# Kernel optimization log

Hardware: AMD Instinct MI355X
Metric: run time of the kernel (lower is better)

The kernel has to match this reference:

```python
import jax, jax.numpy as jnp
import numpy as np

N = 50000        # nodes
E = 800000       # edges (avg degree 16)
F_IN = 256       # cfg.dataset.features
H = 256          # cfg.model.hidden_size


def setup_inputs() -> dict:
    key = jax.random.key(0)
    ks = jax.random.split(key, 8)
    x = jax.random.normal(ks[0], (N, F_IN), dtype=jnp.float32)
    edge_index = jax.random.randint(ks[1], (2, E), 0, N, dtype=jnp.int32)
    # GCNConv weights: layer0 in->hidden, layer1 hidden->hidden, layer2 hidden->1
    W0 = jax.random.normal(ks[2], (F_IN, H), jnp.float32) / np.sqrt(F_IN)
    b0 = jnp.zeros((H,), jnp.float32)
    W1 = jax.random.normal(ks[3], (H, H), jnp.float32) / np.sqrt(H)
    b1 = jnp.zeros((H,), jnp.float32)
    W2 = jax.random.normal(ks[4], (H, 1), jnp.float32) / np.sqrt(H)
    b2 = jnp.zeros((1,), jnp.float32)
    return {"x": x, "edge_index": edge_index, "W0": W0, "b0": b0,
            "W1": W1, "b1": b1, "W2": W2, "b2": b2}


def reference(x, edge_index, W0, b0, W1, b1, W2, b2):
    n = x.shape[0]
    loop = jnp.arange(n, dtype=edge_index.dtype)
    # gcn_norm with self-loops: Ahat = D^{-1/2} (A + I) D^{-1/2}
    src = jnp.concatenate([edge_index[0], loop])  # [E+N]
    dst = jnp.concatenate([edge_index[1], loop])  # [E+N]
    deg = jax.ops.segment_sum(jnp.ones_like(src, dtype=x.dtype), dst, num_segments=n)
    dinv = jnp.where(deg > 0, jax.lax.rsqrt(deg), 0.0)
    norm = dinv[src] * dinv[dst]                  # [E+N]

    def gcn_layer(h, W, b):
        h = h @ W                                              # [N, out]
        agg = jax.ops.segment_sum(norm[:, None] * h[src], dst, num_segments=n)
        return agg + b

    h = jax.nn.relu(gcn_layer(x, W0, b0))
    h = jax.nn.relu(gcn_layer(h, W1, b1))
    return gcn_layer(h, W2, b2)                                # [N, 1]
```

## Files before the change

### kernel.cpp

```cpp
#include <hip/hip_runtime.h>


static inline size_t alignup(size_t x, size_t a) { return (x + a - 1) & ~(a - 1); }

typedef __attribute__((ext_vector_type(8))) short short8;
typedef __attribute__((ext_vector_type(4))) float f32x4;

__device__ inline unsigned short f2bf(float f) {
    union { float f; unsigned int u; } v; v.f = f;
    unsigned int r = v.u + 0x7FFFu + ((v.u >> 16) & 1u);
    return (unsigned short)(r >> 16);
}
__device__ inline float bf2f(unsigned short u) {
    union { unsigned int u; float f; } v; v.u = ((unsigned int)u) << 16;
    return v.f;
}

__global__ __launch_bounds__(256) void k_fill_i32(int* __restrict__ p, int v, int n) {
    int i = blockIdx.x * 256 + threadIdx.x;
    if (i < n) p[i] = v;
}

__global__ __launch_bounds__(256) void k_count_deg(const int* __restrict__ dst, int* __restrict__ deg, int E) {
    int e = blockIdx.x * 256 + threadIdx.x;
    if (e < E) atomicAdd(&deg[dst[e]], 1);
}

__global__ __launch_bounds__(256) void k_scan1(const int* __restrict__ deg, int* __restrict__ rs,
                                               int* __restrict__ bsum, float* __restrict__ dinv, int n) {
    __shared__ int sd[256];
    int b = blockIdx.x, tid = threadIdx.x;
    int base = b * 1024 + tid * 4;
    int v[4];
#pragma unroll
    for (int j = 0; j < 4; ++j) v[j] = (base + j < n) ? deg[base + j] : 0;
    int tot = v[0] + v[1] + v[2] + v[3];
    sd[tid] = tot;
    for (int off = 1; off < 256; off <<= 1) {
        __syncthreads();
        int t = (tid >= off) ? sd[tid - off] : 0;
        __syncthreads();
        sd[tid] += t;
    }
    __syncthreads();
    int run = tid ? sd[tid - 1] : 0;
#pragma unroll
    for (int j = 0; j < 4; ++j) {
        if (base + j < n) {
            rs[base + j] = run;
            dinv[base + j] = rsqrtf((float)v[j] + 1.0f);
        }
        run += v[j];
    }
    if (tid == 255) bsum[b] = sd[255];
}

__global__ __launch_bounds__(256) void k_scan2(int* __restrict__ bsum, int nb) {
    __shared__ int sd[256];
    int tid = threadIdx.x;
    sd[tid] = (tid < nb) ? bsum[tid] : 0;
    for (int off = 1; off < 256; off <<= 1) {
        __syncthreads();
        int t = (tid >= off) ? sd[tid - off] : 0;
        __syncthreads();
        sd[tid] += t;
    }
    __syncthreads();
    if (tid < nb) bsum[tid] = tid ? sd[tid - 1] : 0;
}

__global__ __launch_bounds__(256) void k_scan3(int* __restrict__ rs, int* __restrict__ cursor,
                                               const int* __restrict__ bsum, int n, int E) {
    int b = blockIdx.x, tid = threadIdx.x;
    int off = bsum[b];
    int base = b * 1024 + tid * 4;
#pragma unroll
    for (int j = 0; j < 4; ++j) {
        int idx = base + j;
        if (idx < n) {
            int v = rs[idx] + off;
            rs[idx] = v;
            cursor[idx] = v;
        }
    }
    if (b == 0 && tid == 0) rs[n] = E;
}

__global__ __launch_bounds__(256) void k_fill_csr(const int* __restrict__ src, const int* __restrict__ dst,
                                                  int* __restrict__ cursor, int* __restrict__ col, int E) {
    int e = blockIdx.x * 256 + threadIdx.x;
    if (e < E) {
        int d = dst[e];
        int pos = atomicAdd(&cursor[d], 1);
        col[pos] = src[e];
    }
}

__global__ __launch_bounds__(256) void k_wt2(const float* __restrict__ W0, const float* __restrict__ W1,
                                             unsigned short* __restrict__ Wt0, unsigned short* __restrict__ Wt1) {
    int idx = blockIdx.x * 256 + threadIdx.x;
    const float* W = (idx < 65536) ? W0 : W1;
    unsigned short* Wt = (idx < 65536) ? Wt0 : Wt1;
    int id = idx & 65535;
    int k = id >> 8, n = id & 255;
    Wt[(size_t)n * 256 + k] = f2bf(W[(size_t)k * 256 + n]);
}

__global__ __launch_bounds__(256) void k_xb(const float* __restrict__ x, unsigned short* __restrict__ xb,
                                            int total8) {
    int i = blockIdx.x * 256 + threadIdx.x;
    if (i >= total8) return;
    float4 f0 = *(const float4*)(x + (size_t)i * 8);
    float4 f1 = *(const float4*)(x + (size_t)i * 8 + 4);
    short8 u;
    u[0] = (short)f2bf(f0.x); u[1] = (short)f2bf(f0.y);
    u[2] = (short)f2bf(f0.z); u[3] = (short)f2bf(f0.w);
    u[4] = (short)f2bf(f1.x); u[5] = (short)f2bf(f1.y);
    u[6] = (short)f2bf(f1.z); u[7] = (short)f2bf(f1.w);
    *(short8*)(xb + (size_t)i * 8) = u;
}

__global__ __launch_bounds__(256) void k_gemm_mfma(const unsigned short* __restrict__ A,
                                                   const unsigned short* __restrict__ Wt,
                                                   unsigned short* __restrict__ C,
                                                   const float* __restrict__ dinv, int N) {
    __shared__ __align__(16) unsigned short As2[128 * 32];
    __shared__ __align__(16) unsigned short Bs2[128 * 32];
    __shared__ __align__(16) unsigned short Cs[4 * 64 * 64];

    int tid = threadIdx.x;
    int lane = tid & 63, w = tid >> 6;
    int wr = w >> 1, wc = w & 1;
    int row0 = blockIdx.y * 128, col0 = blockIdx.x * 128;

    f32x4 acc[4][4];
#pragma unroll
    for (int m = 0; m < 4; ++m)
#pragma unroll
        for (int n = 0; n < 4; ++n) acc[m][n] = (f32x4)0.f;

    for (int k0 = 0; k0 < 256; k0 += 32) {
#pragma unroll
        for (int it = 0; it < 2; ++it) {
            int c = tid + it * 256;
            int r = c >> 2, kg = c & 3;
            int grow = row0 + r;
            short8 u = {0, 0, 0, 0, 0, 0, 0, 0};
            if (grow < N) u = *(const short8*)(A + (size_t)grow * 256 + k0 + kg * 8);
            *(short8*)&As2[(r >> 4) * 512 + kg * 128 + (r & 15) * 8] = u;
        }
#pragma unroll
        for (int it = 0; it < 2; ++it) {
            int c = tid + it * 256;
            int n = c >> 2, kg = c & 3;
            short8 u = *(const short8*)(Wt + (size_t)(col0 + n) * 256 + k0 + kg * 8);
            *(short8*)&Bs2[(n >> 4) * 512 + kg * 128 + (n & 15) * 8] = u;
        }
        __syncthreads();
        short8 af[4], bfr[4];
#pragma unroll
        for (int m = 0; m < 4; ++m)
            af[m] = *(const short8*)&As2[(wr * 4 + m) * 512 + (lane >> 4) * 128 + (lane & 15) * 8];
#pragma unroll
        for (int n = 0; n < 4; ++n)
            bfr[n] = *(const short8*)&Bs2[(wc * 4 + n) * 512 + (lane >> 4) * 128 + (lane & 15) * 8];
#pragma unroll
        for (int m = 0; m < 4; ++m)
#pragma unroll
            for (int n = 0; n < 4; ++n)
                acc[m][n] = __builtin_amdgcn_mfma_f32_16x16x32_bf16(af[m], bfr[n], acc[m][n], 0, 0, 0);
        __syncthreads();
    }

    unsigned short* myCs = &Cs[w * 4096];
#pragma unroll
    for (int m = 0; m < 4; ++m) {
#pragma unroll
        for (int j = 0; j < 4; ++j) {
            int r = m * 16 + (lane >> 4) * 4 + j;
            int grow = row0 + wr * 64 + r;
            float d = (grow < N) ? dinv[grow] : 0.f;
#pragma unroll
            for (int n = 0; n < 4; ++n)
                myCs[r * 64 + n * 16 + (lane & 15)] = f2bf(acc[m][n][j] * d);
        }
    }
    __syncthreads();
#pragma unroll
    for (int i = 0; i < 8; ++i) {
        int r = i * 8 + (lane >> 3);
        int grow = row0 + wr * 64 + r;
        if (grow < N) {
            short8 v = *(const short8*)&myCs[r * 64 + (lane & 7) * 8];
            *(short8*)(C + (size_t)grow * 256 + col0 + wc * 64 + (lane & 7) * 8) = v;
        }
    }
}

__global__ __launch_bounds__(256) void k_agg(const unsigned short* __restrict__ t,
                                             unsigned short* __restrict__ h,
                                             const int* __restrict__ rs, const int* __restrict__ col,
                                             const float* __restrict__ dinv, const float* __restrict__ bias,
                                             int N, int do_relu) {
    int wid = (blockIdx.x * 256 + threadIdx.x) >> 6;
    int lane = threadIdx.x & 63;
    if (wid >= N) return;
    int half = lane >> 5, sub = lane & 31;
    const short8* tp = (const short8*)t;

    short8 sv = tp[(size_t)wid * 32 + sub];
    float hsel = (half == 0) ? 1.f : 0.f;
    float a[8];
#pragma unroll
    for (int i = 0; i < 8; ++i) a[i] = hsel * bf2f((unsigned short)sv[i]);

    int e0 = rs[wid], e1 = rs[wid + 1];
    for (int base = e0; base < e1; base += 64) {
        int m = e1 - base; if (m > 64) m = 64;
        int c = (base + lane < e1) ? col[base + lane] : 0;
        int npairs = (m + 1) >> 1;
        int j = 0;
        for (; j + 4 <= npairs; j += 4) {
            int i0 = 2 * j + half, i1 = i0 + 2, i2 = i0 + 4, i3 = i0 + 6;
            int s0 = __shfl(c, i0), s1 = __shfl(c, i1), s2 = __shfl(c, i2), s3 = __shfl(c, i3);
            float f0 = (i0 < m) ? 1.f : 0.f, f1 = (i1 < m) ? 1.f : 0.f;
            float f2 = (i2 < m) ? 1.f : 0.f, f3 = (i3 < m) ? 1.f : 0.f;
            short8 w0 = tp[(size_t)s0 * 32 + sub];
            short8 w1 = tp[(size_t)s1 * 32 + sub];
            short8 w2 = tp[(size_t)s2 * 32 + sub];
            short8 w3 = tp[(size_t)s3 * 32 + sub];
#pragma unroll
            for (int i = 0; i < 8; ++i) {
                a[i] = fmaf(f0, bf2f((unsigned short)w0[i]), a[i]);
                a[i] = fmaf(f1, bf2f((unsigned short)w1[i]), a[i]);
                a[i] = fmaf(f2, bf2f((unsigned short)w2[i]), a[i]);
                a[i] = fmaf(f3, bf2f((unsigned short)w3[i]), a[i]);
            }
        }
        for (; j < npairs; ++j) {
            int i0 = 2 * j + half;
            int s0 = __shfl(c, i0);
            float f0 = (i0 < m) ? 1.f : 0.f;
            short8 w0 = tp[(size_t)s0 * 32 + sub];
#pragma unroll
            for (int i = 0; i < 8; ++i) a[i] = fmaf(f0, bf2f((unsigned short)w0[i]), a[i]);
        }
    }
#pragma unroll
    for (int i = 0; i < 8; ++i) a[i] += __shfl_xor(a[i], 32, 64);

    if (half == 0) {
        float d = dinv[wid];
        float4 b0 = ((const float4*)bias)[sub * 2];
        float4 b1 = ((const float4*)bias)[sub * 2 + 1];
        float o[8];
        o[0] = fmaf(d, a[0], b0.x); o[1] = fmaf(d, a[1], b0.y);
        o[2] = fmaf(d, a[2], b0.z); o[3] = fmaf(d, a[3], b0.w);
        o[4] = fmaf(d, a[4], b1.x); o[5] = fmaf(d, a[5], b1.y);
        o[6] = fmaf(d, a[6], b1.z); o[7] = fmaf(d, a[7], b1.w);
        short8 u;
#pragma unroll
        for (int i = 0; i < 8; ++i) {
            float v = do_relu ? fmaxf(o[i], 0.f) : o[i];
            u[i] = (short)f2bf(v);
        }
        *(short8*)(h + (size_t)wid * 256 + sub * 8) = u;
    }
}

__global__ __launch_bounds__(256) void k_gemv(const unsigned short* __restrict__ h, const float* __restrict__ w,
                                              const float* __restrict__ dinv, float* __restrict__ z, int N) {
    int wid = (blockIdx.x * 256 + threadIdx.x) >> 6;
    int lane = threadIdx.x & 63;
    if (wid >= N) return;
    ushort4 hv = ((const ushort4*)(h + (size_t)wid * 256))[lane];
    float4 wv = ((const float4*)w)[lane];
    float s = bf2f(hv.x) * wv.x + bf2f(hv.y) * wv.y + bf2f(hv.z) * wv.z + bf2f(hv.w) * wv.w;
#pragma unroll
    for (int off = 32; off > 0; off >>= 1) s += __shfl_down(s, off, 64);
    if (lane == 0) z[wid] = dinv[wid] * s;
}

__global__ __launch_bounds__(256) void k_agg_out(const float* __restrict__ z, float* __restrict__ out,
                                                 const int* __restrict__ rs, const int* __restrict__ col,
                                                 const float* __restrict__ dinv, const float* __restrict__ b2,
                                                 int N) {
    int wid = (blockIdx.x * 256 + threadIdx.x) >> 6;
    int lane = threadIdx.x & 63;
    if (wid >= N) return;
    int e0 = rs[wid], e1 = rs[wid + 1];
    float v = 0.f;
    for (int base = e0; base < e1; base += 64) {
        int e = base + lane;
        if (e < e1) v += z[col[e]];
    }
#pragma unroll
    for (int off = 32; off > 0; off >>= 1) v += __shfl_down(v, off, 64);
    if (lane == 0) out[wid] = fmaf(dinv[wid], v + z[wid], b2[0]);
}

extern "C" void kernel_launch(void* const* d_in, const int* in_sizes, int n_in,
                              void* d_out, int out_size, void* d_ws, size_t ws_size,
                              hipStream_t stream) {
    const float* x  = (const float*)d_in[0];
    const int*   ei = (const int*)d_in[1];
    const float* W0 = (const float*)d_in[2];
    const float* b0 = (const float*)d_in[3];
    const float* W1 = (const float*)d_in[4];
    const float* b1 = (const float*)d_in[5];
    const float* W2 = (const float*)d_in[6];
    const float* b2 = (const float*)d_in[7];
    float* out = (float*)d_out;

    int N = in_sizes[0] / 256;
    int E = in_sizes[1] / 2;
    const int* esrc = ei;
    const int* edst = ei + E;

    char* p = (char*)d_ws;
    unsigned short* tb = (unsigned short*)p; p += alignup((size_t)N * 256 * 2, 16);
    unsigned short* hb = (unsigned short*)p; p += alignup((size_t)N * 256 * 2, 16);
    unsigned short* xb = (unsigned short*)p; p += alignup((size_t)N * 256 * 2, 16);
    unsigned short* Wt0 = (unsigned short*)p; p += 256 * 256 * 2;
    unsigned short* Wt1 = (unsigned short*)p; p += 256 * 256 * 2;
    float* z = (float*)p;      p += alignup((size_t)N * 4, 16);
    float* dinv = (float*)p;   p += alignup((size_t)N * 4, 16);
    int* deg = (int*)p;        p += alignup((size_t)N * 4, 16);
    int* cursor = (int*)p;     p += alignup((size_t)N * 4, 16);
    int* rs = (int*)p;         p += alignup((size_t)(N + 1) * 4, 16);
    int* col = (int*)p;        p += alignup((size_t)E * 4, 16);
    int* bsum = (int*)p;       p += 256 * 4;

    int nb = (N + 1023) / 1024;
    dim3 blk(256);

    k_fill_i32<<<(N + 255) / 256, blk, 0, stream>>>(deg, 0, N);
    k_count_deg<<<(E + 255) / 256, blk, 0, stream>>>(edst, deg, E);
    k_scan1<<<nb, blk, 0, stream>>>(deg, rs, bsum, dinv, N);
    k_scan2<<<1, blk, 0, stream>>>(bsum, nb);
    k_scan3<<<nb, blk, 0, stream>>>(rs, cursor, bsum, N, E);
    k_fill_csr<<<(E + 255) / 256, blk, 0, stream>>>(esrc, edst, cursor, col, E);
    k_wt2<<<512, blk, 0, stream>>>(W0, W1, Wt0, Wt1);
    int total8 = N * 32;
    k_xb<<<(total8 + 255) / 256, blk, 0, stream>>>(x, xb, total8);

    dim3 gg(2, (N + 127) / 128);
    k_gemm_mfma<<<gg, blk, 0, stream>>>(xb, Wt0, tb, dinv, N);
    k_agg<<<(N + 3) / 4, blk, 0, stream>>>(tb, hb, rs, col, dinv, b0, N, 1);
    k_gemm_mfma<<<gg, blk, 0, stream>>>(hb, Wt1, tb, dinv, N);
    k_agg<<<(N + 3) / 4, blk, 0, stream>>>(tb, hb, rs, col, dinv, b1, N, 1);
    k_gemv<<<(N + 3) / 4, blk, 0, stream>>>(hb, W2, dinv, z, N);
    k_agg_out<<<(N + 3) / 4, blk, 0, stream>>>(z, out, rs, col, dinv, b2, N);
}
```

Before: 384.8 us.

## Fuse x bf16 conversion into GEMM, prefetch K tiles, fuse GEMV into aggregation

The separate fp32-to-bf16 conversion kernel is removed; the first GEMM now reads fp32 x and converts it while loading. The GEMM loop prefetches the next K tile into registers during the MFMA work and reuses one shared buffer for staging and output. The second aggregation computes the final 256->1 projection in place, so the second hidden activation is never written and the separate GEMV kernel goes away. This removes a full N×256 bf16 write and read pair plus two launches, at the cost of more registers and an extra barrier per K step.

```diff
diff --git a/kernel.cpp b/kernel.cpp
--- a/kernel.cpp
+++ b/kernel.cpp
@@ -106,27 +106,15 @@
     Wt[(size_t)n * 256 + k] = f2bf(W[(size_t)k * 256 + n]);
 }
 
-__global__ __launch_bounds__(256) void k_xb(const float* __restrict__ x, unsigned short* __restrict__ xb,
-                                            int total8) {
-    int i = blockIdx.x * 256 + threadIdx.x;
-    if (i >= total8) return;
-    float4 f0 = *(const float4*)(x + (size_t)i * 8);
-    float4 f1 = *(const float4*)(x + (size_t)i * 8 + 4);
-    short8 u;
-    u[0] = (short)f2bf(f0.x); u[1] = (short)f2bf(f0.y);
-    u[2] = (short)f2bf(f0.z); u[3] = (short)f2bf(f0.w);
-    u[4] = (short)f2bf(f1.x); u[5] = (short)f2bf(f1.y);
-    u[6] = (short)f2bf(f1.z); u[7] = (short)f2bf(f1.w);
-    *(short8*)(xb + (size_t)i * 8) = u;
-}
-
-__global__ __launch_bounds__(256) void k_gemm_mfma(const unsigned short* __restrict__ A,
+template <bool AF32>
+__global__ __launch_bounds__(256) void k_gemm_mfma(const void* __restrict__ Ap,
                                                    const unsigned short* __restrict__ Wt,
                                                    unsigned short* __restrict__ C,
                                                    const float* __restrict__ dinv, int N) {
-    __shared__ __align__(16) unsigned short As2[128 * 32];
-    __shared__ __align__(16) unsigned short Bs2[128 * 32];
-    __shared__ __align__(16) unsigned short Cs[4 * 64 * 64];
+    __shared__ __align__(16) unsigned short smem[16384];
+    unsigned short* As2 = smem;
+    unsigned short* Bs2 = smem + 4096;
+    unsigned short* Cs = smem;
 
     int tid = threadIdx.x;
     int lane = tid & 63, w = tid >> 6;
@@ -139,24 +127,52 @@
 #pragma unroll
         for (int n = 0; n < 4; ++n) acc[m][n] = (f32x4)0.f;
 
-    for (int k0 = 0; k0 < 256; k0 += 32) {
-#pragma unroll
-        for (int it = 0; it < 2; ++it) {
-            int c = tid + it * 256;
-            int r = c >> 2, kg = c & 3;
-            int grow = row0 + r;
-            short8 u = {0, 0, 0, 0, 0, 0, 0, 0};
-            if (grow < N) u = *(const short8*)(A + (size_t)grow * 256 + k0 + kg * 8);
-            *(short8*)&As2[(r >> 4) * 512 + kg * 128 + (r & 15) * 8] = u;
-        }
-#pragma unroll
-        for (int it = 0; it < 2; ++it) {
-            int c = tid + it * 256;
-            int n = c >> 2, kg = c & 3;
-            short8 u = *(const short8*)(Wt + (size_t)(col0 + n) * 256 + k0 + kg * 8);
-            *(short8*)&Bs2[(n >> 4) * 512 + kg * 128 + (n & 15) * 8] = u;
-        }
-        __syncthreads();
+    const int c0 = tid, c1 = tid + 256;
+    const int ar0 = c0 >> 2, akg0 = c0 & 3, ar1 = c1 >> 2, akg1 = c1 & 3;
+
+    auto loadA = [&](int r, int kg, int k0) -> short8 {
+        short8 u = {0, 0, 0, 0, 0, 0, 0, 0};
+        int grow = row0 + r;
+        if (grow < N) {
+            if constexpr (AF32) {
+                const float* g = (const float*)Ap + (size_t)grow * 256 + k0 + kg * 8;
+                float4 f0 = *(const float4*)g;
+                float4 f1 = *(const float4*)(g + 4);
+                u[0] = (short)f2bf(f0.x); u[1] = (short)f2bf(f0.y);
+                u[2] = (short)f2bf(f0.z); u[3] = (short)f2bf(f0.w);
+                u[4] = (short)f2bf(f1.x); u[5] = (short)f2bf(f1.y);
+                u[6] = (short)f2bf(f1.z); u[7] = (short)f2bf(f1.w);
+            } else {
+                u = *(const short8*)((const unsigned short*)Ap + (size_t)grow * 256 + k0 + kg * 8);
+            }
+        }
+        return u;
+    };
+    auto loadB = [&](int n, int kg, int k0) -> short8 {
+        return *(const short8*)(Wt + (size_t)(col0 + n) * 256 + k0 + kg * 8);
+    };
+    auto stash = [&](short8 a0, short8 a1, short8 b0, short8 b1) {
+        *(short8*)&As2[(ar0 >> 4) * 512 + akg0 * 128 + (ar0 & 15) * 8] = a0;
+        *(short8*)&As2[(ar1 >> 4) * 512 + akg1 * 128 + (ar1 & 15) * 8] = a1;
+        *(short8*)&Bs2[(ar0 >> 4) * 512 + akg0 * 128 + (ar0 & 15) * 8] = b0;
+        *(short8*)&Bs2[(ar1 >> 4) * 512 + akg1 * 128 + (ar1 & 15) * 8] = b1;
+    };
+
+    {
+        short8 a0 = loadA(ar0, akg0, 0), a1 = loadA(ar1, akg1, 0);
+        short8 b0 = loadB(ar0, akg0, 0), b1 = loadB(ar1, akg1, 0);
+        stash(a0, a1, b0, b1);
+    }
+    __syncthreads();
+
+#pragma unroll
+    for (int i = 0; i < 8; ++i) {
+        short8 na0, na1, nb0, nb1;
+        if (i < 7) {
+            int k0 = i * 32 + 32;
+            na0 = loadA(ar0, akg0, k0); na1 = loadA(ar1, akg1, k0);
+            nb0 = loadB(ar0, akg0, k0); nb1 = loadB(ar1, akg1, k0);
+        }
         short8 af[4], bfr[4];
 #pragma unroll
         for (int m = 0; m < 4; ++m)
@@ -169,8 +185,13 @@
 #pragma unroll
             for (int n = 0; n < 4; ++n)
                 acc[m][n] = __builtin_amdgcn_mfma_f32_16x16x32_bf16(af[m], bfr[n], acc[m][n], 0, 0, 0);
-        __syncthreads();
-    }
+        if (i < 7) {
+            __syncthreads();
+            stash(na0, na1, nb0, nb1);
+            __syncthreads();
+        }
+    }
+    __syncthreads();
 
     unsigned short* myCs = &Cs[w * 4096];
 #pragma unroll
@@ -197,11 +218,13 @@
     }
 }
 
+template <bool FUSE_GEMV>
 __global__ __launch_bounds__(256) void k_agg(const unsigned short* __restrict__ t,
                                              unsigned short* __restrict__ h,
                                              const int* __restrict__ rs, const int* __restrict__ col,
                                              const float* __restrict__ dinv, const float* __restrict__ bias,
-                                             int N, int do_relu) {
+                                             const float* __restrict__ W2, float* __restrict__ z,
+                                             int N) {
     int wid = (blockIdx.x * 256 + threadIdx.x) >> 6;
     int lane = threadIdx.x & 63;
     if (wid >= N) return;
@@ -249,36 +272,33 @@
 #pragma unroll
     for (int i = 0; i < 8; ++i) a[i] += __shfl_xor(a[i], 32, 64);
 
-    if (half == 0) {
-        float d = dinv[wid];
-        float4 b0 = ((const float4*)bias)[sub * 2];
-        float4 b1 = ((const float4*)bias)[sub * 2 + 1];
-        float o[8];
-        o[0] = fmaf(d, a[0], b0.x); o[1] = fmaf(d, a[1], b0.y);
-        o[2] = fmaf(d, a[2], b0.z); o[3] = fmaf(d, a[3], b0.w);
-        o[4] = fmaf(d, a[4], b1.x); o[5] = fmaf(d, a[5], b1.y);
-        o[6] = fmaf(d, a[6], b1.z); o[7] = fmaf(d, a[7], b1.w);
-        short8 u;
-#pragma unroll
-        for (int i = 0; i < 8; ++i) {
-            float v = do_relu ? fmaxf(o[i], 0.f) : o[i];
-            u[i] = (short)f2bf(v);
-        }
-        *(short8*)(h + (size_t)wid * 256 + sub * 8) = u;
-    }
-}
-
-__global__ __launch_bounds__(256) void k_gemv(const unsigned short* __restrict__ h, const float* __restrict__ w,
-                                              const float* __restrict__ dinv, float* __restrict__ z, int N) {
-    int wid = (blockIdx.x * 256 + threadIdx.x) >> 6;
-    int lane = threadIdx.x & 63;
-    if (wid >= N) return;
-    ushort4 hv = ((const ushort4*)(h + (size_t)wid * 256))[lane];
-    float4 wv = ((const float4*)w)[lane];
-    float s = bf2f(hv.x) * wv.x + bf2f(hv.y) * wv.y + bf2f(hv.z) * wv.z + bf2f(hv.w) * wv.w;
-#pragma unroll
-    for (int off = 32; off > 0; off >>= 1) s += __shfl_down(s, off, 64);
-    if (lane == 0) z[wid] = dinv[wid] * s;
+    float d = dinv[wid];
+    float4 b0 = ((const float4*)bias)[sub * 2];
+    float4 b1 = ((const float4*)bias)[sub * 2 + 1];
+    float o[8];
+    o[0] = fmaf(d, a[0], b0.x); o[1] = fmaf(d, a[1], b0.y);
+    o[2] = fmaf(d, a[2], b0.z); o[3] = fmaf(d, a[3], b0.w);
+    o[4] = fmaf(d, a[4], b1.x); o[5] = fmaf(d, a[5], b1.y);
+    o[6] = fmaf(d, a[6], b1.z); o[7] = fmaf(d, a[7], b1.w);
+#pragma unroll
+    for (int i = 0; i < 8; ++i) o[i] = fmaxf(o[i], 0.f);
+
+    if constexpr (FUSE_GEMV) {
+        float4 wv0 = ((const float4*)W2)[sub * 2];
+        float4 wv1 = ((const float4*)W2)[sub * 2 + 1];
+        float zp = o[0] * wv0.x + o[1] * wv0.y + o[2] * wv0.z + o[3] * wv0.w +
+                   o[4] * wv1.x + o[5] * wv1.y + o[6] * wv1.z + o[7] * wv1.w;
+#pragma unroll
+        for (int off = 16; off > 0; off >>= 1) zp += __shfl_down(zp, off, 32);
+        if (lane == 0) z[wid] = d * zp;
+    } else {
+        if (half == 0) {
+            short8 u;
+#pragma unroll
+            for (int i = 0; i < 8; ++i) u[i] = (short)f2bf(o[i]);
+            *(short8*)(h + (size_t)wid * 256 + sub * 8) = u;
+        }
+    }
 }
 
 __global__ __launch_bounds__(256) void k_agg_out(const float* __restrict__ z, float* __restrict__ out,
@@ -320,7 +340,6 @@
     char* p = (char*)d_ws;
     unsigned short* tb = (unsigned short*)p; p += alignup((size_t)N * 256 * 2, 16);
     unsigned short* hb = (unsigned short*)p; p += alignup((size_t)N * 256 * 2, 16);
-    unsigned short* xb = (unsigned short*)p; p += alignup((size_t)N * 256 * 2, 16);
     unsigned short* Wt0 = (unsigned short*)p; p += 256 * 256 * 2;
     unsigned short* Wt1 = (unsigned short*)p; p += 256 * 256 * 2;
     float* z = (float*)p;      p += alignup((size_t)N * 4, 16);
@@ -341,14 +360,11 @@
     k_scan3<<<nb, blk, 0, stream>>>(rs, cursor, bsum, N, E);
     k_fill_csr<<<(E + 255) / 256, blk, 0, stream>>>(esrc, edst, cursor, col, E);
     k_wt2<<<512, blk, 0, stream>>>(W0, W1, Wt0, Wt1);
-    int total8 = N * 32;
-    k_xb<<<(total8 + 255) / 256, blk, 0, stream>>>(x, xb, total8);
 
     dim3 gg(2, (N + 127) / 128);
-    k_gemm_mfma<<<gg, blk, 0, stream>>>(xb, Wt0, tb, dinv, N);
-    k_agg<<<(N + 3) / 4, blk, 0, stream>>>(tb, hb, rs, col, dinv, b0, N, 1);
-    k_gemm_mfma<<<gg, blk, 0, stream>>>(hb, Wt1, tb, dinv, N);
-    k_agg<<<(N + 3) / 4, blk, 0, stream>>>(tb, hb, rs, col, dinv, b1, N, 1);
-    k_gemv<<<(N + 3) / 4, blk, 0, stream>>>(hb, W2, dinv, z, N);
+    k_gemm_mfma<true><<<gg, blk, 0, stream>>>(x, Wt0, tb, dinv, N);
+    k_agg<false><<<(N + 3) / 4, blk, 0, stream>>>(tb, hb, rs, col, dinv, b0, nullptr, nullptr, N);
+    k_gemm_mfma<false><<<gg, blk, 0, stream>>>(hb, Wt1, tb, dinv, N);
+    k_agg<true><<<(N + 3) / 4, blk, 0, stream>>>(tb, nullptr, rs, col, dinv, b1, W2, z, N);
     k_agg_out<<<(N + 3) / 4, blk, 0, stream>>>(z, out, rs, col, dinv, b2, N);
 }
```

Measured after the change: 361.8 us. 1.06x faster.
